# Kernel optimization log

Hardware: AMD Instinct MI355X
Metric: run time of the kernel (lower is better)

Reference implementation:

```python
import jax, jax.numpy as jnp
import numpy as np

D = 768; HID = 3072; FFN = 2048; NH = 8; NL = 2; T = 64; V = 50257; B = 16
ALPHA = 0.4; HD = D // NH

def _gelu(x):
    return jax.nn.gelu(x, approximate=False)

def _ln(x, g, b, eps=1e-5):
    m = x.mean(-1, keepdims=True)
    v = x.var(-1, keepdims=True)
    return (x - m) / jnp.sqrt(v + eps) * g + b

def _l2norm(x):
    return x / jnp.maximum(jnp.linalg.norm(x, axis=-1, keepdims=True), 1e-12)

def _mha(x, in_w, in_b, out_w, out_b, mask):
    b, t, _ = x.shape
    qkv = x @ in_w.T + in_b
    q, k, v = jnp.split(qkv, 3, axis=-1)
    q = q.reshape(b, t, NH, HD); k = k.reshape(b, t, NH, HD); v = v.reshape(b, t, NH, HD)
    s = jnp.einsum('bqhd,bkhd->bhqk', q, k) / jnp.sqrt(jnp.asarray(HD, jnp.float32))
    s = jnp.where(mask[None, None], -jnp.inf, s)
    a = jax.nn.softmax(s, axis=-1)
    o = jnp.einsum('bhqk,bkhd->bqhd', a, v).reshape(b, t, D)
    return o @ out_w.T + out_b

def _forward(token_ids, emb, pos_emb, attn_in_w, attn_in_b, attn_out_w, attn_out_b,
             ff_w1, ff_b1, ff_w2, ff_b2, n1_g, n1_b, n2_g, n2_b, enc_norm_g, enc_norm_b,
             V0, b0, V1, b1, cp_w1, cp_b1, cp_w2, cp_b2, gate_w, gate_b, temp_w, R,
             out_g, out_b, lm_head):
    sg = jax.lax.stop_gradient
    x = emb[token_ids] + pos_emb[None, :token_ids.shape[1]]
    t = token_ids.shape[1]
    mask = jnp.triu(jnp.ones((t, t), bool), 1)
    for l in range(NL):
        xn = _ln(x, n1_g[l], n1_b[l])
        x = x + _mha(xn, attn_in_w[l], attn_in_b[l], attn_out_w[l], attn_out_b[l], mask)
        xn = _ln(x, n2_g[l], n2_b[l])
        x = x + _gelu(xn @ ff_w1[l].T + ff_b1[l]) @ ff_w2[l].T + ff_b2[l]
    ctx = _l2norm(_ln(x, enc_norm_g, enc_norm_b))  # [B,T,D]

    def step(h_prev, ctx_t):
        h_d = sg(h_prev)                      # h_prev.detach()
        traw = h_d @ R                        # temporal_raw
        tc = ctx_t + ALPHA * traw             # temporal_context
        # differentiable shadow path through hierarchy weights V0,b0,V1,b1
        h_sh = _gelu(tc @ V0 + b0)
        core_sh = _l2norm(_gelu(h_sh @ V1 + b1))
        # settled state: hierarchy inference under no_grad (settle approximated
        # by the same feedforward pass; fully stop-gradiented like x.detach())
        tcd = sg(tc)
        core_set = sg(_l2norm(_gelu(_gelu(tcd @ V0 + b0) @ V1 + b1)))
        blend = 0.5 * core_sh + 0.5 * core_set
        cf = _gelu(blend @ cp_w1.T + cp_b1) @ cp_w2.T + cp_b2   # core_proj
        tf = traw @ temp_w.T                                     # temporal_proj
        gate = jax.nn.sigmoid(jnp.concatenate([ctx_t, cf], -1) @ gate_w.T + gate_b)
        h_t = gate * (cf + ALPHA * tf) + (1.0 - gate) * ctx_t    # gate_warmup=1.0
        h_t = jnp.clip(_ln(h_t, out_g, out_b), -5.0, 5.0)
        return sg(h_t), h_t @ lm_head.T

    h0 = jnp.zeros((token_ids.shape[0], D), jnp.float32)
    _, logits = jax.lax.scan(step, h0, jnp.swapaxes(ctx, 0, 1))
    return jnp.transpose(logits, (1, 0, 2))

def setup_inputs():
    key = jax.random.key(0)
    ks = iter(jax.random.split(key, 64))
    def nrm(shape, s=0.02):
        return jax.random.normal(next(ks), shape, jnp.float32) * s
    return {
        'token_ids': jax.random.randint(next(ks), (B, T), 0, V),
        'emb': nrm((V, D)),
        'pos_emb': nrm((T, D)),
        'attn_in_w': nrm((NL, 3 * D, D)),
        'attn_in_b': jnp.zeros((NL, 3 * D), jnp.float32),
        'attn_out_w': nrm((NL, D, D)),
        'attn_out_b': jnp.zeros((NL, D), jnp.float32),
        'ff_w1': nrm((NL, FFN, D)),
        'ff_b1': jnp.zeros((NL, FFN), jnp.float32),
        'ff_w2': nrm((NL, D, FFN)),
        'ff_b2': jnp.zeros((NL, D), jnp.float32),
        'n1_g': jnp.ones((NL, D), jnp.float32),
        'n1_b': jnp.zeros((NL, D), jnp.float32),
        'n2_g': jnp.ones((NL, D), jnp.float32),
        'n2_b': jnp.zeros((NL, D), jnp.float32),
        'enc_norm_g': jnp.ones((D,), jnp.float32),
        'enc_norm_b': jnp.zeros((D,), jnp.float32),
        'V0': nrm((D, HID)),
        'b0': jnp.zeros((HID,), jnp.float32),
        'V1': nrm((HID, D)),
        'b1': jnp.zeros((D,), jnp.float32),
        'cp_w1': nrm((D, D)),
        'cp_b1': jnp.zeros((D,), jnp.float32),
        'cp_w2': nrm((D, D)),
        'cp_b2': jnp.zeros((D,), jnp.float32),
        'gate_w': nrm((D, 2 * D)),
        'gate_b': jnp.zeros((D,), jnp.float32),
        'temp_w': nrm((D, D)),
        'R': nrm((D, D), 0.1),
        'out_g': jnp.ones((D,), jnp.float32),
        'out_b': jnp.zeros((D,), jnp.float32),
        'lm_head': nrm((V, D)),
    }

def reference(token_ids, emb, pos_emb, attn_in_w, attn_in_b, attn_out_w, attn_out_b,
              ff_w1, ff_b1, ff_w2, ff_b2, n1_g, n1_b, n2_g, n2_b, enc_norm_g, enc_norm_b,
              V0, b0, V1, b1, cp_w1, cp_b1, cp_w2, cp_b2, gate_w, gate_b, temp_w, R,
              out_g, out_b, lm_head):
    return _forward(token_ids, emb, pos_emb, attn_in_w, attn_in_b, attn_out_w, attn_out_b,
                    ff_w1, ff_b1, ff_w2, ff_b2, n1_g, n1_b, n2_g, n2_b, enc_norm_g, enc_norm_b,
                    V0, b0, V1, b1, cp_w1, cp_b1, cp_w2, cp_b2, gate_w, gate_b, temp_w, R,
                    out_g, out_b, lm_head)
```

## Files before the change

### kernel.cpp

```cpp
#include <hip/hip_runtime.h>
#include <math.h>

typedef _Float16 f16;
typedef f16 f16x8 __attribute__((ext_vector_type(8)));
typedef f16 f16x4 __attribute__((ext_vector_type(4)));
typedef float f32x4 __attribute__((ext_vector_type(4)));
typedef unsigned int u32;
typedef unsigned long long u64;

#define TT 64
#define DD 768
#define MR 1024
#define ALPHAF 0.4f
#define NWG 120
#define GRID 240
#define LMN 50257
#define LMK 768

__device__ __forceinline__ float geluf(float x){
  return 0.5f*x*(1.0f + erff(x*0.70710678118654752f));
}

__device__ __forceinline__ u64 ld_a64(const void* p){
  return __hip_atomic_load((const u64*)p, __ATOMIC_RELAXED, __HIP_MEMORY_SCOPE_AGENT);
}
__device__ __forceinline__ f16x8 ld_act16h(const f16* p){
  union { u64 u[2]; f16x8 v; } c;
  c.u[0] = ld_a64(p); c.u[1] = ld_a64(p + 4); return c.v;
}
__device__ __forceinline__ float ld_actf(const float* p){
  union { u32 u; float f; } c;
  c.u = __hip_atomic_load((const u32*)p, __ATOMIC_RELAXED, __HIP_MEMORY_SCOPE_AGENT);
  return c.f;
}
__device__ __forceinline__ void st_actf(float* p, float v){
  union { u32 u; float f; } c; c.f = v;
  __hip_atomic_store((u32*)p, c.u, __ATOMIC_RELAXED, __HIP_MEMORY_SCOPE_AGENT);
}
__device__ __forceinline__ void st_acth(f16* p, float v){
  union { unsigned short u; f16 h; } c; c.h = (f16)v;
  __hip_atomic_store((unsigned short*)p, c.u, __ATOMIC_RELAXED, __HIP_MEMORY_SCOPE_AGENT);
}

__device__ __forceinline__ void egbar(int* ef, int ep){
  __syncthreads();
  if (threadIdx.x == 0){
    __threadfence();
    __hip_atomic_store(ef + blockIdx.x*32, ep, __ATOMIC_RELAXED, __HIP_MEMORY_SCOPE_AGENT);
  }
  {
    int id = threadIdx.x; bool active = id < GRID;
    const int* fp = ef + id*32;
    while (true){
      int v = active ? __hip_atomic_load(fp, __ATOMIC_RELAXED, __HIP_MEMORY_SCOPE_AGENT) : ep;
      if (__ballot(v >= ep) == ~0ull) break;
      __builtin_amdgcn_s_sleep(1);
    }
  }
  __syncthreads();
  if (threadIdx.x == 0) __threadfence();
  __syncthreads();
}

__device__ __forceinline__ void postf(int* f, int ep){
  asm volatile("s_waitcnt vmcnt(0)" ::: "memory");
  __syncthreads();
  if (threadIdx.x == 0)
    __hip_atomic_store(f, ep, __ATOMIC_RELAXED, __HIP_MEMORY_SCOPE_AGENT);
}
__device__ __forceinline__ void waitf(const int* f, int n, int ep){
  if (threadIdx.x < 64){
    int lane = threadIdx.x;
    while (true){
      bool ok = true;
      for (int i = lane; i < n; i += 64){
        if (__hip_atomic_load(f + i*32, __ATOMIC_RELAXED, __HIP_MEMORY_SCOPE_AGENT) < ep){
          ok = false; break;
        }
      }
      if (__ballot(ok) == ~0ull) break;
      __builtin_amdgcn_s_sleep(1);
    }
  }
  __syncthreads();
}

__device__ __forceinline__ void red_store(float* rb, int lane, f32x4 a){
  rb[lane] = a[0]; rb[64+lane] = a[1]; rb[128+lane] = a[2]; rb[192+lane] = a[3];
}
__device__ __forceinline__ f32x4 red_sum4(float rb[4][256], int lane){
  f32x4 s;
  #pragma unroll
  for (int r = 0; r < 4; r++)
    s[r] = rb[0][r*64+lane] + rb[1][r*64+lane] + rb[2][r*64+lane] + rb[3][r*64+lane];
  return s;
}
__device__ __forceinline__ f32x4 red_sum2(float rb[4][256], int lane, int w0, int w1){
  f32x4 s;
  #pragma unroll
  for (int r = 0; r < 4; r++)
    s[r] = rb[w0][r*64+lane] + rb[w1][r*64+lane];
  return s;
}

__device__ void dev_ln(const float* xr, const float* g, const float* b,
                       float* outr, float* outTr, float* red, bool l2n){
  int tid = threadIdx.x, lane = tid & 63, wid = tid >> 6;
  float v[3]; float s = 0.f, ss = 0.f;
  #pragma unroll
  for (int j = 0; j < 3; j++){ float t0 = xr[tid + j*256]; v[j] = t0; s += t0; ss += t0*t0; }
  #pragma unroll
  for (int o = 1; o < 64; o <<= 1){ s += __shfl_xor(s, o); ss += __shfl_xor(ss, o); }
  if (lane == 0){ red[wid] = s; red[4+wid] = ss; }
  __syncthreads();
  s  = red[0]+red[1]+red[2]+red[3];
  ss = red[4]+red[5]+red[6]+red[7];
  float mean = s*(1.f/768.f);
  float var  = ss*(1.f/768.f) - mean*mean;
  float rstd = rsqrtf(var + 1e-5f);
  float y[3];
  #pragma unroll
  for (int j = 0; j < 3; j++){ int n = tid + j*256; y[j] = (v[j]-mean)*rstd*g[n] + b[n]; }
  if (l2n){
    float n2 = y[0]*y[0] + y[1]*y[1] + y[2]*y[2];
    #pragma unroll
    for (int o = 1; o < 64; o <<= 1) n2 += __shfl_xor(n2, o);
    __syncthreads();
    if (lane == 0) red[wid] = n2;
    __syncthreads();
    n2 = red[0]+red[1]+red[2]+red[3];
    float inv = 1.f / fmaxf(sqrtf(n2), 1e-12f);
    y[0] *= inv; y[1] *= inv; y[2] *= inv;
  }
  #pragma unroll
  for (int j = 0; j < 3; j++) outr[tid + j*256] = y[j];
  if (outTr){
    #pragma unroll
    for (int j = 0; j < 3; j++) outTr[tid + j*256] = y[j];
  }
  __syncthreads();
}

__device__ void dev_gemm_tile(char* lds, const float* A, int lda,
    const float* Bw, int ldb, int nrb, int N, int K, int m0, int n0,
    const float* bias, const float* res, float* outF, f16* outH,
    float scale, int act, int operm)
{
  int tid = threadIdx.x;
  int lane = tid & 63, wid = tid >> 6;
  int wr = (wid >> 1)*64, wc = (wid & 1)*64;
  int l15 = lane & 15, kb = lane >> 4;
  f32x4 acc[4][4];
  #pragma unroll
  for (int i = 0; i < 4; i++)
    #pragma unroll
    for (int j = 0; j < 4; j++){ f32x4 z = {0.f,0.f,0.f,0.f}; acc[i][j] = z; }
  int rA = tid >> 3;
  int k4 = (tid & 7)*4;
  float4 va[4], vb[4];
  #pragma unroll
  for (int it = 0; it < 4; ++it){
    int r = it*32 + rA;
    va[it] = *(const float4*)(A + (size_t)(m0+r)*lda + k4);
    int rB = n0 + r;
    if (rB < nrb) vb[it] = *(const float4*)(Bw + (size_t)rB*ldb + k4);
    else { vb[it].x=0.f; vb[it].y=0.f; vb[it].z=0.f; vb[it].w=0.f; }
  }
  for (int kk = 0; kk < K; kk += 32){
    char* cb = lds + (((kk >> 5) & 1) ? 20480 : 0);
    f16 (*As)[40] = (f16(*)[40])cb;
    f16 (*Bs)[40] = (f16(*)[40])(cb + 10240);
    #pragma unroll
    for (int it = 0; it < 4; ++it){
      int r = it*32 + rA;
      *(f16x4*)(&As[r][k4]) = (f16x4){(f16)va[it].x,(f16)va[it].y,(f16)va[it].z,(f16)va[it].w};
      *(f16x4*)(&Bs[r][k4]) = (f16x4){(f16)vb[it].x,(f16)vb[it].y,(f16)vb[it].z,(f16)vb[it].w};
    }
    __syncthreads();
    if (kk + 32 < K){
      #pragma unroll
      for (int it = 0; it < 4; ++it){
        int r = it*32 + rA;
        va[it] = *(const float4*)(A + (size_t)(m0+r)*lda + kk + 32 + k4);
        int rB = n0 + r;
        if (rB < nrb) vb[it] = *(const float4*)(Bw + (size_t)rB*ldb + kk + 32 + k4);
        else { vb[it].x=0.f; vb[it].y=0.f; vb[it].z=0.f; vb[it].w=0.f; }
      }
    }
    f16x8 af[4], bfv[4];
    #pragma unroll
    for (int i = 0; i < 4; i++) af[i]  = *(const f16x8*)(&As[wr + i*16 + l15][kb*8]);
    #pragma unroll
    for (int j = 0; j < 4; j++) bfv[j] = *(const f16x8*)(&Bs[wc + j*16 + l15][kb*8]);
    #pragma unroll
    for (int i = 0; i < 4; i++)
      #pragma unroll
      for (int j = 0; j < 4; j++)
        acc[i][j] = __builtin_amdgcn_mfma_f32_16x16x32_f16(af[i], bfv[j], acc[i][j], 0, 0, 0);
  }
  __syncthreads();
  #pragma unroll
  for (int i = 0; i < 4; i++){
    #pragma unroll
    for (int j = 0; j < 4; j++){
      #pragma unroll
      for (int r = 0; r < 4; r++){
        int m = m0 + wr + i*16 + kb*4 + r;
        int n = n0 + wc + j*16 + l15;
        if (n < N){
          float v = acc[i][j][r]*scale;
          if (bias) v += bias[n];
          if (act == 1) v = geluf(v);
          if (res) v += res[(size_t)m*N + n];
          size_t off;
          if (operm == 0) off = (size_t)m*N + n;
          else            off = ((size_t)(m & 63)*16 + (m >> 6))*N + n;
          if (outF) outF[off] = v;
          if (outH) outH[off] = (f16)v;
        }
      }
    }
  }
}

__device__ void dev_attn(char* lds, const float* qkv, float* o, int bh){
  float (*kv)[96] = (float(*)[96])lds;
  float (*sm)[68] = (float(*)[68])(lds + 24576);
  int b = bh >> 3, h = bh & 7;
  int tid = threadIdx.x;
  const float* base = qkv + (size_t)b*64*2304 + h*96;
  for (int idx = tid; idx < 64*96; idx += 256){ int i = idx/96, d = idx - i*96;
    kv[i][d] = base[(size_t)i*2304 + 768 + d]; }
  __syncthreads();
  {
    int i = tid >> 2;
    const float* q = base + (size_t)i*2304;
    int j0 = (tid & 3)*16;
    for (int jj = 0; jj < 16; jj++){
      int j = j0 + jj;
      float sv = -1e30f;
      if (j <= i){ float acc = 0.f;
        for (int d = 0; d < 96; d++) acc += q[d]*kv[j][d];
        sv = acc*0.10206207261596576f; }
      sm[i][j] = sv;
    }
  }
  __syncthreads();
  for (int idx = tid; idx < 64*96; idx += 256){ int i = idx/96, d = idx - i*96;
    kv[i][d] = base[(size_t)i*2304 + 1536 + d]; }
  if (tid < 64){
    int i = tid;
    float mx = -1e30f;
    for (int j = 0; j <= i; j++) mx = fmaxf(mx, sm[i][j]);
    float sum = 0.f;
    for (int j = 0; j <= i; j++){ float e = expf(sm[i][j]-mx); sm[i][j] = e; sum += e; }
    float inv = 1.f/sum;
    for (int j = 0; j <= i; j++) sm[i][j] *= inv;
  }
  __syncthreads();
  for (int idx = tid; idx < 64*96; idx += 256){
    int i = idx/96, d = idx - i*96;
    float acc = 0.f;
    for (int j = 0; j <= i; j++) acc += sm[i][j]*kv[j][d];
    o[(size_t)(b*64+i)*768 + h*96 + d] = acc;
  }
  __syncthreads();
}

__device__ void dev_tr_f(char* lds, const float* in, float* out, int R, int C, int bx, int by){
  float (*tile)[33] = (float(*)[33])lds;
  int r0 = by*32, c0 = bx*32;
  int tx = threadIdx.x & 31, ty = threadIdx.x >> 5;
  #pragma unroll
  for (int i = 0; i < 32; i += 8) tile[ty+i][tx] = in[(size_t)(r0+ty+i)*C + (c0+tx)];
  __syncthreads();
  #pragma unroll
  for (int i = 0; i < 32; i += 8) out[(size_t)(c0+ty+i)*R + (r0+tx)] = tile[tx][ty+i];
  __syncthreads();
}
__device__ void dev_tr_h(char* lds, const float* in, f16* out, int R, int C, int bx, int by){
  float (*tile)[33] = (float(*)[33])lds;
  int r0 = by*32, c0 = bx*32;
  int tx = threadIdx.x & 31, ty = threadIdx.x >> 5;
  #pragma unroll
  for (int i = 0; i < 32; i += 8) tile[ty+i][tx] = in[(size_t)(r0+ty+i)*C + (c0+tx)];
  __syncthreads();
  #pragma unroll
  for (int i = 0; i < 32; i += 8) out[(size_t)(c0+ty+i)*R + (r0+tx)] = (f16)tile[tx][ty+i];
  __syncthreads();
}

__global__ void k_init(int* flags){
  for (int i = threadIdx.x; i < 512*32; i += 256) flags[i] = 0;
}

__global__ __launch_bounds__(256, 1) void k_all(
  const int* tok, const float* emb, const float* pos,
  const float* aiw, const float* aib, const float* aow, const float* aob,
  const float* fw1, const float* fb1, const float* fw2, const float* fb2,
  const float* n1g, const float* n1b, const float* n2g, const float* n2b,
  const float* eng, const float* enb,
  const float* V0, const float* b0, const float* V1, const float* b1,
  const float* cw1, const float* cb1, const float* cw2, const float* cb2,
  const float* gw, const float* gb_, const float* tw, const float* Rm,
  const float* og, const float* ob, const float* lmw,
  float* x, float* xn, float* qkv, float* o_, float* mid,
  float* ctx, float* ctxT, float* V0t, float* cw2t,
  float* ctxV0T, float* gctxT, float* bdg,
  f16* WAf, f16* V1tf, f16* Wc1f, f16* WDf, f16* lmw16,
  f16* hf, f16* h1f, f16* c1f, f16* gcaf,
  float* cf, float* gpre, float* tfs, int* flags, float* out)
{
  __shared__ __align__(16) char smem[147456];
  __shared__ float redbuf[4][256];
  __shared__ float normp[4][16];
  __shared__ float red[8];
  const int tid = threadIdx.x, lane = tid & 63, wid = tid >> 6;
  const int bid = blockIdx.x;
  const int l15 = lane & 15, kb = lane >> 4;
  int* afl = flags;
  int* bfl = flags + 120*32;
  int* cfl = flags + 168*32;
  int* dfl = flags + 192*32;
  int* mfl = flags + 240*32;
  int* encf = flags + 256*32;
  int eep = 0;

  for (int m = bid; m < MR; m += GRID){
    int t = m & 63; int id = tok[m];
    const float* e = emb + (size_t)id*DD;
    const float* p = pos + (size_t)t*DD;
    float* xr = x + (size_t)m*DD;
    for (int j = tid; j < DD; j += 256) xr[j] = e[j] + p[j];
  }
  egbar(encf, ++eep);

  for (int l = 0; l < 2; l++){
    for (int m = bid; m < MR; m += GRID)
      dev_ln(x + (size_t)m*DD, n1g + l*DD, n1b + l*DD, xn + (size_t)m*DD, nullptr, red, false);
    egbar(encf, ++eep);
    for (int tl = bid; tl < 144; tl += GRID)
      dev_gemm_tile(smem, xn, 768, aiw + (size_t)l*2304*768, 768, 2304, 2304, 768,
                    (tl % 8)*128, (tl / 8)*128, aib + l*2304, nullptr, qkv, nullptr, 1.f, 0, 0);
    egbar(encf, ++eep);
    for (int u = bid; u < 128; u += GRID) dev_attn(smem, qkv, o_, u);
    egbar(encf, ++eep);
    for (int tl = bid; tl < 48; tl += GRID)
      dev_gemm_tile(smem, o_, 768, aow + (size_t)l*768*768, 768, 768, 768, 768,
                    (tl % 8)*128, (tl / 8)*128, aob + l*768, x, x, nullptr, 1.f, 0, 0);
    egbar(encf, ++eep);
    for (int m = bid; m < MR; m += GRID)
      dev_ln(x + (size_t)m*DD, n2g + l*DD, n2b + l*DD, xn + (size_t)m*DD, nullptr, red, false);
    egbar(encf, ++eep);
    for (int tl = bid; tl < 128; tl += GRID)
      dev_gemm_tile(smem, xn, 768, fw1 + (size_t)l*2048*768, 768, 2048, 2048, 768,
                    (tl % 8)*128, (tl / 8)*128, fb1 + l*2048, nullptr, mid, nullptr, 1.f, 1, 0);
    egbar(encf, ++eep);
    for (int tl = bid; tl < 48; tl += GRID)
      dev_gemm_tile(smem, mid, 2048, fw2 + (size_t)l*768*2048, 2048, 768, 768, 2048,
                    (tl % 8)*128, (tl / 8)*128, fb2 + l*768, x, x, nullptr, 1.f, 0, 0);
    egbar(encf, ++eep);
  }
  for (int m = bid; m < MR; m += GRID)
    dev_ln(x + (size_t)m*DD, eng, enb, ctx + (size_t)m*DD,
           ctxT + ((size_t)(m & 63)*16 + (m >> 6))*DD, red, true);
  egbar(encf, ++eep);

  for (int task = bid; task < 5184; task += GRID){
    if (task < 2304)      dev_tr_f(smem, V0, V0t, 768, 3072, task % 96, task / 96);
    else if (task < 2880){ int t2 = task - 2304; dev_tr_f(smem, cw2, cw2t, 768, 768, t2 % 24, t2 / 24); }
    else                 { int t2 = task - 2880; dev_tr_h(smem, V1, V1tf, 3072, 768, t2 % 24, t2 / 24); }
  }
  {
    const int g0 = bid*256 + tid, stride = GRID*256;
    for (int i = g0; i < 73728; i += stride){
      float4 a = ((const float4*)cw1)[i*2]; float4 b2 = ((const float4*)cw1)[i*2+1];
      ((f16x8*)Wc1f)[i] = (f16x8){(f16)a.x,(f16)a.y,(f16)a.z,(f16)a.w,(f16)b2.x,(f16)b2.y,(f16)b2.z,(f16)b2.w};
    }
    for (int i = g0; i < 73728; i += stride){
      float4 a = ((const float4*)cw2)[i*2]; float4 b2 = ((const float4*)cw2)[i*2+1];
      ((f16x8*)WDf)[i] = (f16x8){(f16)a.x,(f16)a.y,(f16)a.z,(f16)a.w,(f16)b2.x,(f16)b2.y,(f16)b2.z,(f16)b2.w};
    }
    for (int g = g0; g < 768; g += stride){
      const float* row = gw + (size_t)g*1536 + 768;
      float s = 0.f;
      for (int j = 0; j < 768; j++) s += cb2[j]*row[j];
      bdg[g] = s;
    }
  }
  egbar(encf, ++eep);

  for (int task = bid; task < 456; task += GRID){
    if (task < 144)
      dev_gemm_tile(smem, V0t, 768, Rm, 768, 768, 768, 768,
                    (task % 24)*128, (task / 24)*128, nullptr, nullptr, nullptr, WAf, ALPHAF, 0, 0);
    else if (task < 180){ int t2 = task - 144;
      dev_gemm_tile(smem, tw, 768, Rm, 768, 768, 768, 768,
                    (t2 % 6)*128, (t2 / 6)*128, nullptr, nullptr, nullptr, WAf + (size_t)3072*768, ALPHAF, 0, 0); }
    else if (task < 372){ int t2 = task - 180;
      dev_gemm_tile(smem, ctx, 768, V0t, 768, 3072, 3072, 768,
                    (t2 % 8)*128, (t2 / 8)*128, b0, nullptr, ctxV0T, nullptr, 1.f, 0, 1); }
    else if (task < 420){ int t2 = task - 372;
      dev_gemm_tile(smem, ctx, 768, gw, 1536, 768, 768, 768,
                    (t2 % 8)*128, (t2 / 8)*128, nullptr, nullptr, gctxT, nullptr, 1.f, 0, 1); }
    else { int t2 = task - 420;
      dev_gemm_tile(smem, gw + 768, 1536, cw2t, 768, 768, 768, 768,
                    (t2 % 6)*128, (t2 / 6)*128, nullptr, nullptr, nullptr, WDf + (size_t)768*768, 1.f, 0, 0); }
  }
  egbar(encf, ++eep);

  if (bid >= NWG){
    const int lw = bid - NWG;
    const int wr = (wid >> 1)*64, wc = (wid & 1)*64;
    for (int nt = lw; nt < 393; nt += 120){
      int r0 = nt*128;
      int rend = r0 + 128; if (rend > LMN) rend = LMN;
      int u0 = r0*96, u1 = rend*96;
      for (int i = u0 + tid; i < u1; i += 256){
        float4 a = ((const float4*)lmw)[(size_t)i*2];
        float4 b2 = ((const float4*)lmw)[(size_t)i*2+1];
        ((f16x8*)lmw16)[i] = (f16x8){(f16)a.x,(f16)a.y,(f16)a.z,(f16)a.w,
                                     (f16)b2.x,(f16)b2.y,(f16)b2.z,(f16)b2.w};
      }
    }
    __syncthreads();
    for (int q = 0; q < 8; ++q){
      waitf(mfl, 16, q*8 + 8);
      size_t arow[4];
      #pragma unroll
      for (int i = 0; i < 4; i++){
        int rl = wr + i*16 + l15;
        arow[i] = ((size_t)(rl >> 3)*TT + q*8 + (rl & 7))*DD + kb*8;
      }
      for (int nt = lw; nt < 393; nt += 120){
        int n0 = nt*128;
        size_t brow[4];
        #pragma unroll
        for (int j = 0; j < 4; j++){
          int n = n0 + wc + j*16 + l15;
          if (n > LMN-1) n = LMN-1;
          brow[j] = (size_t)n*LMK + kb*8;
        }
        f32x4 acc[4][4];
        #pragma unroll
        for (int i = 0; i < 4; i++)
          #pragma unroll
          for (int j = 0; j < 4; j++){ f32x4 z = {0.f,0.f,0.f,0.f}; acc[i][j] = z; }
        #pragma unroll 4
        for (int kk = 0; kk < LMK; kk += 32){
          f16x8 af[4], bf[4];
          #pragma unroll
          for (int i = 0; i < 4; i++) af[i] = ld_act16h(hf + arow[i] + kk);
          #pragma unroll
          for (int j = 0; j < 4; j++) bf[j] = *(const f16x8*)(lmw16 + brow[j] + kk);
          #pragma unroll
          for (int i = 0; i < 4; i++)
            #pragma unroll
            for (int j = 0; j < 4; j++)
              acc[i][j] = __builtin_amdgcn_mfma_f32_16x16x32_f16(af[i], bf[j], acc[i][j], 0, 0, 0);
        }
        #pragma unroll
        for (int i = 0; i < 4; i++){
          #pragma unroll
          for (int j = 0; j < 4; j++){
            #pragma unroll
            for (int r = 0; r < 4; r++){
              int ml = wr + i*16 + kb*4 + r;
              int b = ml >> 3, tt = q*8 + (ml & 7);
              int n = n0 + wc + j*16 + l15;
              if (n < LMN) out[((size_t)b*TT + tt)*LMN + n] = acc[i][j][r];
            }
          }
        }
      }
    }
    return;
  }

  {
    const f16* src = WAf + (size_t)bid*32*768;
    for (int c = tid; c < 3072; c += 256){
      int row = c/96, kc = c - row*96;
      int off = (row*1536 + kc*16) ^ ((row&7)<<4);
      *(f16x8*)(smem + off) = *(const f16x8*)(src + (size_t)row*768 + kc*8);
    }
    if (bid < 48){
      const f16* s2 = V1tf + (size_t)bid*16*3072;
      for (int c = tid; c < 6144; c += 256){
        int row = c/384, kc = c - row*384;
        int off = (row*6144 + kc*16) ^ ((row&7)<<4);
        *(f16x8*)(smem + 49152 + off) = *(const f16x8*)(s2 + (size_t)row*3072 + kc*8);
      }
    } else if (bid < 72){
      const f16* s2 = Wc1f + (size_t)(bid-48)*32*768;
      for (int c = tid; c < 3072; c += 256){
        int row = c/96, kc = c - row*96;
        int off = (row*1536 + kc*16) ^ ((row&7)<<4);
        *(f16x8*)(smem + 49152 + off) = *(const f16x8*)(s2 + (size_t)row*768 + kc*8);
      }
    } else {
      const f16* s2 = WDf + (size_t)(bid-72)*32*768;
      for (int c = tid; c < 3072; c += 256){
        int row = c/96, kc = c - row*96;
        int off = (row*1536 + kc*16) ^ ((row&7)<<4);
        *(f16x8*)(smem + 49152 + off) = *(const f16x8*)(s2 + (size_t)row*768 + kc*8);
      }
    }
  }
  __syncthreads();

  const int n_a = bid*32 + (wid>>1)*16 + l15;
  float b1v = 0.f;
  if (bid < 48) b1v = b1[bid*16 + l15];
  float cpb1v = 0.f;
  if (bid >= 48 && bid < 72) cpb1v = cb1[((bid-48)*2 + (wid>>1))*16 + l15];
  float dbv = 0.f; int n_d = 0;
  if (bid >= 72){
    n_d = ((bid-72)*2 + (wid>>1))*16 + l15;
    dbv = (n_d < 768) ? cb2[n_d] : bdg[n_d - 768];
  }
  float gb3[3], og3[3], ob3[3];
  if (bid < 16){
    #pragma unroll
    for (int j = 0; j < 3; j++){
      int n = tid + j*256;
      gb3[j] = gb_[n]; og3[j] = og[n]; ob3[j] = ob[n];
    }
  }

  for (int t = 0; t < TT; ++t){
    const int ep = t + 1;
    f32x4 cv = {0.f,0.f,0.f,0.f};
    if ((wid & 1) == 0 && n_a < 3072){
      const float* p = ctxV0T + (size_t)t*16*3072 + n_a;
      #pragma unroll
      for (int r = 0; r < 4; r++) cv[r] = p[(size_t)(kb*4+r)*3072];
    }

    if (t > 0) waitf(mfl, 16, t);
    {
      const int u = wid >> 1, kh = wid & 1;
      const int k0 = kh*384 + kb*8;
      f32x4 a = {0.f,0.f,0.f,0.f};
      if (t > 0){
        const f16* ap = hf + ((size_t)l15*TT + (t-1))*DD + k0;
        const int row = u*16 + l15, rowoff = row*1536, sw = (row&7)<<4;
        #pragma unroll
        for (int b = 0; b < 12; b++){
          int wb = (rowoff + (k0 + b*32)*2) ^ sw;
          f16x8 vb = *(const f16x8*)(smem + wb);
          f16x8 va = ld_act16h(ap + b*32);
          a = __builtin_amdgcn_mfma_f32_16x16x32_f16(va, vb, a, 0,0,0);
        }
      }
      red_store(redbuf[wid], lane, a);
    }
    __syncthreads();
    if ((wid & 1) == 0){
      f32x4 s4 = red_sum2(redbuf, lane, wid, wid+1);
      #pragma unroll
      for (int r = 0; r < 4; r++){
        int m = kb*4 + r;
        if (n_a < 3072){
          float hv = geluf(s4[r] + cv[r]);
          st_acth(h1f + (size_t)m*3072 + n_a, hv);
        } else {
          st_actf(tfs + m*DD + (n_a - 3072), s4[r]);
        }
      }
    }
    postf(afl + bid*32, ep);
    if (bid < 48){
      waitf(afl, 120, ep);
      const int k0 = wid*768 + kb*8;
      const f16* ap = h1f + (size_t)l15*3072 + k0;
      const int rowoff = l15*6144, sw = (l15&7)<<4;
      f32x4 a = {0.f,0.f,0.f,0.f};
      #pragma unroll
      for (int b = 0; b < 24; b++){
        int wb = (rowoff + (k0 + b*32)*2) ^ sw;
        f16x8 vb = *(const f16x8*)(smem + 49152 + wb);
        f16x8 va = ld_act16h(ap + b*32);
        a = __builtin_amdgcn_mfma_f32_16x16x32_f16(va, vb, a, 0,0,0);
      }
      red_store(redbuf[wid], lane, a);
      __syncthreads();
      if (wid == 0){
        f32x4 s4 = red_sum4(redbuf, lane);
        int n = bid*16 + l15;
        #pragma unroll
        for (int r = 0; r < 4; r++){
          int m = kb*4 + r;
          st_acth(c1f + (size_t)m*DD + n, geluf(s4[r] + b1v));
        }
      }
      postf(bfl + bid*32, ep);
    }
    float gv[3], cxv[3];
    if (bid < 16){
      #pragma unroll
      for (int j = 0; j < 3; j++){
        size_t o2 = ((size_t)t*16 + bid)*DD + tid + j*256;
        gv[j] = gctxT[o2]; cxv[j] = ctxT[o2];
      }
    }
    if (bid >= 48 && bid < 72){
      waitf(bfl, 48, ep);
      const int u = wid >> 1, kh = wid & 1;
      const int k0 = kh*384 + kb*8;
      const f16* ap = c1f + (size_t)l15*DD + k0;
      const int row = u*16 + l15, rowoff = row*1536, sw = (row&7)<<4;
      f32x4 a = {0.f,0.f,0.f,0.f};
      float sq = 0.f;
      #pragma unroll
      for (int b = 0; b < 12; b++){
        int wb = (rowoff + (k0 + b*32)*2) ^ sw;
        f16x8 vb = *(const f16x8*)(smem + 49152 + wb);
        f16x8 va = ld_act16h(ap + b*32);
        a = __builtin_amdgcn_mfma_f32_16x16x32_f16(va, vb, a, 0,0,0);
        #pragma unroll
        for (int j = 0; j < 8; j++){ float xv = (float)va[j]; sq = fmaf(xv, xv, sq); }
      }
      sq += __shfl_xor(sq,16); sq += __shfl_xor(sq,32);
      if (lane < 16) normp[wid][lane] = sq;
      red_store(redbuf[wid], lane, a);
      __syncthreads();
      if ((wid & 1) == 0){
        f32x4 s4 = red_sum2(redbuf, lane, wid, wid+1);
        int n = ((bid-48)*2 + (wid>>1))*16 + l15;
        #pragma unroll
        for (int r = 0; r < 4; r++){
          int m = kb*4 + r;
          float nm = normp[wid][m] + normp[wid+1][m];
          float inv = 1.f / fmaxf(sqrtf(nm), 1e-12f);
          st_acth(gcaf + (size_t)m*DD + n, geluf(s4[r]*inv + cpb1v));
        }
      }
      postf(cfl + (bid-48)*32, ep);
    }
    if (bid >= 72){
      waitf(cfl, 24, ep);
      const int u = wid >> 1, kh = wid & 1;
      const int k0 = kh*384 + kb*8;
      const f16* ap = gcaf + (size_t)l15*DD + k0;
      const int row = u*16 + l15, rowoff = row*1536, sw = (row&7)<<4;
      f32x4 a = {0.f,0.f,0.f,0.f};
      #pragma unroll
      for (int b = 0; b < 12; b++){
        int wb = (rowoff + (k0 + b*32)*2) ^ sw;
        f16x8 vb = *(const f16x8*)(smem + 49152 + wb);
        f16x8 va = ld_act16h(ap + b*32);
        a = __builtin_amdgcn_mfma_f32_16x16x32_f16(va, vb, a, 0,0,0);
      }
      red_store(redbuf[wid], lane, a);
      __syncthreads();
      if ((wid & 1) == 0){
        f32x4 s4 = red_sum2(redbuf, lane, wid, wid+1);
        #pragma unroll
        for (int r = 0; r < 4; r++){
          int m = kb*4 + r;
          if (n_d < 768) st_actf(cf + m*DD + n_d, s4[r] + dbv);
          else           st_actf(gpre + m*DD + (n_d - 768), s4[r] + dbv);
        }
      }
      postf(dfl + (bid-72)*32, ep);
    }
    if (bid < 16){
      waitf(dfl, 48, ep);
      int m = bid;
      float vals[3]; float s = 0.f, ss = 0.f;
      #pragma unroll
      for (int j = 0; j < 3; j++){
        int n = tid + j*256;
        float gi = gv[j] + ld_actf(gpre + m*DD + n) + gb3[j];
        float gate = 1.f/(1.f + expf(-gi));
        float v = gate*(ld_actf(cf + m*DD + n) + ld_actf(tfs + m*DD + n)) + (1.f - gate)*cxv[j];
        vals[j] = v; s += v; ss += v*v;
      }
      #pragma unroll
      for (int o2 = 1; o2 < 64; o2 <<= 1){ s += __shfl_xor(s, o2); ss += __shfl_xor(ss, o2); }
      if (lane == 0){ red[wid] = s; red[4+wid] = ss; }
      __syncthreads();
      s  = red[0]+red[1]+red[2]+red[3];
      ss = red[4]+red[5]+red[6]+red[7];
      float mean = s*(1.f/768.f), var = ss*(1.f/768.f) - mean*mean;
      float rstd = rsqrtf(var + 1e-5f);
      #pragma unroll
      for (int j = 0; j < 3; j++){
        int n = tid + j*256;
        float y = (vals[j]-mean)*rstd*og3[j] + ob3[j];
        y = fminf(5.f, fmaxf(-5.f, y));
        st_acth(hf + ((size_t)m*TT + t)*DD + n, y);
      }
      postf(mfl + bid*32, ep);
    }
  }
}

extern "C" void kernel_launch(void* const* d_in, const int* in_sizes, int n_in,
                              void* d_out, int out_size, void* d_ws, size_t ws_size,
                              hipStream_t stream)
{
  (void)in_sizes; (void)n_in; (void)out_size; (void)ws_size;
  const int*   tok = (const int*)d_in[0];
  const float* emb = (const float*)d_in[1];
  const float* pos = (const float*)d_in[2];
  const float* aiw = (const float*)d_in[3];
  const float* aib = (const float*)d_in[4];
  const float* aow = (const float*)d_in[5];
  const float* aob = (const float*)d_in[6];
  const float* fw1 = (const float*)d_in[7];
  const float* fb1 = (const float*)d_in[8];
  const float* fw2 = (const float*)d_in[9];
  const float* fb2 = (const float*)d_in[10];
  const float* n1g = (const float*)d_in[11];
  const float* n1b = (const float*)d_in[12];
  const float* n2g = (const float*)d_in[13];
  const float* n2b = (const float*)d_in[14];
  const float* eng = (const float*)d_in[15];
  const float* enb = (const float*)d_in[16];
  const float* V0  = (const float*)d_in[17];
  const float* b0  = (const float*)d_in[18];
  const float* V1  = (const float*)d_in[19];
  const float* b1  = (const float*)d_in[20];
  const float* cw1 = (const float*)d_in[21];
  const float* cb1 = (const float*)d_in[22];
  const float* cw2 = (const float*)d_in[23];
  const float* cb2 = (const float*)d_in[24];
  const float* gw  = (const float*)d_in[25];
  const float* gb  = (const float*)d_in[26];
  const float* tw  = (const float*)d_in[27];
  const float* Rm  = (const float*)d_in[28];
  const float* og  = (const float*)d_in[29];
  const float* ob  = (const float*)d_in[30];
  const float* lmw = (const float*)d_in[31];
  float* out = (float*)d_out;

  char* base = (char*)d_ws; size_t off = 0;
  auto alloc = [&](size_t bytes)->void*{
    off = (off + 255) & ~(size_t)255; void* p = base + off; off += bytes; return p; };

  float* x     = (float*)alloc((size_t)MR*DD*4);
  float* xn    = (float*)alloc((size_t)MR*DD*4);
  float* qkv   = (float*)alloc((size_t)MR*2304*4);
  float* o_    = (float*)alloc((size_t)MR*DD*4);
  float* mid   = (float*)alloc((size_t)MR*2048*4);
  float* ctx   = (float*)alloc((size_t)MR*DD*4);
  float* ctxT  = (float*)alloc((size_t)MR*DD*4);
  float* V0t   = (float*)alloc((size_t)3072*768*4);
  float* cw2t  = (float*)alloc((size_t)768*768*4);
  float* ctxV0T= (float*)alloc((size_t)MR*3072*4);
  float* gctxT = (float*)alloc((size_t)MR*DD*4);
  float* bdg   = (float*)alloc(768*4);
  f16*   WAf   = (f16*)alloc((size_t)3840*768*2);
  f16*   V1tf  = (f16*)alloc((size_t)768*3072*2);
  f16*   Wc1f  = (f16*)alloc((size_t)768*768*2);
  f16*   WDf   = (f16*)alloc((size_t)1536*768*2);
  f16*   lmw16 = (f16*)alloc((size_t)LMN*768*2);
  f16*   hf    = (f16*)alloc((size_t)MR*DD*2);
  f16*   h1f   = (f16*)alloc((size_t)16*3072*2);
  f16*   c1f   = (f16*)alloc((size_t)16*768*2);
  f16*   gcaf  = (f16*)alloc((size_t)16*768*2);
  float* cf    = (float*)alloc((size_t)16*768*4);
  float* gpre  = (float*)alloc((size_t)16*768*4);
  float* tfs   = (float*)alloc((size_t)16*768*4);
  int*   flags = (int*)alloc((size_t)512*32*4);

  k_init<<<1, 256, 0, stream>>>(flags);
  k_all<<<GRID, 256, 0, stream>>>(tok, emb, pos, aiw, aib, aow, aob,
      fw1, fb1, fw2, fb2, n1g, n1b, n2g, n2b, eng, enb,
      V0, b0, V1, b1, cw1, cb1, cw2, cb2, gw, gb, tw, Rm, og, ob, lmw,
      x, xn, qkv, o_, mid, ctx, ctxT, V0t, cw2t, ctxV0T, gctxT, bdg,
      WAf, V1tf, Wc1f, WDf, lmw16, hf, h1f, c1f, gcaf, cf, gpre, tfs, flags, out);
}
```

Measured before the change: 2.698 ms.

## Fuse LayerNorm into GEMM A-loads and split-K the FFN down-projection

Replaces the materialized LayerNorm passes with per-row mean/rstd statistics, which are applied while loading A tiles in the QKV and FFN1 GEMMs. Stats for the first LN are computed during embedding. The FFN2 GEMM is split four ways over K into partial buffers, giving 192 tiles instead of 48 to fill the 240-block grid. A finish pass sums the partials with the residual and bias, computes the next stats, and for the last layer folds in the final norm plus L2 normalization. It also changes one flag index in the recurrent phase from block id to row id. The intent is fewer grid barriers and less xn traffic, at the cost of extra partial-sum memory traffic and per-element normalize work inside the GEMM load loop.

```diff
diff --git a/kernel.cpp b/kernel.cpp
--- a/kernel.cpp
+++ b/kernel.cpp
@@ -103,12 +103,11 @@
   return s;
 }
 
-__device__ void dev_ln(const float* xr, const float* g, const float* b,
-                       float* outr, float* outTr, float* red, bool l2n){
+__device__ void dev_rowstats(const float* xr, float* red, float2* outstat){
   int tid = threadIdx.x, lane = tid & 63, wid = tid >> 6;
-  float v[3]; float s = 0.f, ss = 0.f;
-  #pragma unroll
-  for (int j = 0; j < 3; j++){ float t0 = xr[tid + j*256]; v[j] = t0; s += t0; ss += t0*t0; }
+  float s = 0.f, ss = 0.f;
+  #pragma unroll
+  for (int j = 0; j < 3; j++){ float t0 = xr[tid + j*256]; s += t0; ss += t0*t0; }
   #pragma unroll
   for (int o = 1; o < 64; o <<= 1){ s += __shfl_xor(s, o); ss += __shfl_xor(ss, o); }
   if (lane == 0){ red[wid] = s; red[4+wid] = ss; }
@@ -116,27 +115,56 @@
   s  = red[0]+red[1]+red[2]+red[3];
   ss = red[4]+red[5]+red[6]+red[7];
   float mean = s*(1.f/768.f);
-  float var  = ss*(1.f/768.f) - mean*mean;
-  float rstd = rsqrtf(var + 1e-5f);
+  float rstd = rsqrtf(ss*(1.f/768.f) - mean*mean + 1e-5f);
+  if (tid == 0){ outstat->x = mean; outstat->y = rstd; }
+  __syncthreads();
+}
+
+__device__ void dev_ff2_finish(const float* pfb, const float* bias, float* x, int m,
+    float* red, float2* outstat, bool finalln,
+    const float* g, const float* b, float* ctx, float* ctxT){
+  int tid = threadIdx.x, lane = tid & 63, wid = tid >> 6;
+  float* xr = x + (size_t)m*DD;
+  float v[3]; float s = 0.f, ss = 0.f;
+  #pragma unroll
+  for (int j = 0; j < 3; j++){
+    int n = tid + j*256;
+    size_t o = (size_t)m*DD + n;
+    float t0 = xr[n] + bias[n] + pfb[o] + pfb[(size_t)MR*DD + o]
+             + pfb[2*(size_t)MR*DD + o] + pfb[3*(size_t)MR*DD + o];
+    xr[n] = t0; v[j] = t0; s += t0; ss += t0*t0;
+  }
+  #pragma unroll
+  for (int o = 1; o < 64; o <<= 1){ s += __shfl_xor(s, o); ss += __shfl_xor(ss, o); }
+  if (lane == 0){ red[wid] = s; red[4+wid] = ss; }
+  __syncthreads();
+  s  = red[0]+red[1]+red[2]+red[3];
+  ss = red[4]+red[5]+red[6]+red[7];
+  float mean = s*(1.f/768.f);
+  float rstd = rsqrtf(ss*(1.f/768.f) - mean*mean + 1e-5f);
+  if (!finalln){
+    if (tid == 0){ outstat->x = mean; outstat->y = rstd; }
+    __syncthreads();
+    return;
+  }
   float y[3];
   #pragma unroll
   for (int j = 0; j < 3; j++){ int n = tid + j*256; y[j] = (v[j]-mean)*rstd*g[n] + b[n]; }
-  if (l2n){
-    float n2 = y[0]*y[0] + y[1]*y[1] + y[2]*y[2];
-    #pragma unroll
-    for (int o = 1; o < 64; o <<= 1) n2 += __shfl_xor(n2, o);
-    __syncthreads();
-    if (lane == 0) red[wid] = n2;
-    __syncthreads();
-    n2 = red[0]+red[1]+red[2]+red[3];
-    float inv = 1.f / fmaxf(sqrtf(n2), 1e-12f);
-    y[0] *= inv; y[1] *= inv; y[2] *= inv;
-  }
-  #pragma unroll
-  for (int j = 0; j < 3; j++) outr[tid + j*256] = y[j];
-  if (outTr){
-    #pragma unroll
-    for (int j = 0; j < 3; j++) outTr[tid + j*256] = y[j];
+  float n2 = y[0]*y[0] + y[1]*y[1] + y[2]*y[2];
+  #pragma unroll
+  for (int o = 1; o < 64; o <<= 1) n2 += __shfl_xor(n2, o);
+  __syncthreads();
+  if (lane == 0) red[wid] = n2;
+  __syncthreads();
+  n2 = red[0]+red[1]+red[2]+red[3];
+  float inv = 1.f / fmaxf(sqrtf(n2), 1e-12f);
+  float* cT = ctxT + ((size_t)(m & 63)*16 + (m >> 6))*DD;
+  #pragma unroll
+  for (int j = 0; j < 3; j++){
+    int n = tid + j*256;
+    float yy = y[j]*inv;
+    ctx[(size_t)m*DD + n] = yy;
+    cT[n] = yy;
   }
   __syncthreads();
 }
@@ -144,7 +172,8 @@
 __device__ void dev_gemm_tile(char* lds, const float* A, int lda,
     const float* Bw, int ldb, int nrb, int N, int K, int m0, int n0,
     const float* bias, const float* res, float* outF, f16* outH,
-    float scale, int act, int operm)
+    float scale, int act, int operm,
+    const float2* lnstats, const float* lng, const float* lnb)
 {
   int tid = threadIdx.x;
   int lane = tid & 63, wid = tid >> 6;
@@ -157,7 +186,14 @@
     for (int j = 0; j < 4; j++){ f32x4 z = {0.f,0.f,0.f,0.f}; acc[i][j] = z; }
   int rA = tid >> 3;
   int k4 = (tid & 7)*4;
+  float2 msr[4];
+  if (lnstats){
+    #pragma unroll
+    for (int it = 0; it < 4; ++it) msr[it] = lnstats[m0 + it*32 + rA];
+  }
   float4 va[4], vb[4];
+  float4 g4, b4;
+  if (lnstats){ g4 = *(const float4*)(lng + k4); b4 = *(const float4*)(lnb + k4); }
   #pragma unroll
   for (int it = 0; it < 4; ++it){
     int r = it*32 + rA;
@@ -166,6 +202,16 @@
     if (rB < nrb) vb[it] = *(const float4*)(Bw + (size_t)rB*ldb + k4);
     else { vb[it].x=0.f; vb[it].y=0.f; vb[it].z=0.f; vb[it].w=0.f; }
   }
+  if (lnstats){
+    #pragma unroll
+    for (int it = 0; it < 4; ++it){
+      float mn = msr[it].x, rs = msr[it].y;
+      va[it].x = (va[it].x-mn)*rs*g4.x + b4.x;
+      va[it].y = (va[it].y-mn)*rs*g4.y + b4.y;
+      va[it].z = (va[it].z-mn)*rs*g4.z + b4.z;
+      va[it].w = (va[it].w-mn)*rs*g4.w + b4.w;
+    }
+  }
   for (int kk = 0; kk < K; kk += 32){
     char* cb = lds + (((kk >> 5) & 1) ? 20480 : 0);
     f16 (*As)[40] = (f16(*)[40])cb;
@@ -178,6 +224,7 @@
     }
     __syncthreads();
     if (kk + 32 < K){
+      if (lnstats){ g4 = *(const float4*)(lng + kk + 32 + k4); b4 = *(const float4*)(lnb + kk + 32 + k4); }
       #pragma unroll
       for (int it = 0; it < 4; ++it){
         int r = it*32 + rA;
@@ -185,6 +232,16 @@
         int rB = n0 + r;
         if (rB < nrb) vb[it] = *(const float4*)(Bw + (size_t)rB*ldb + kk + 32 + k4);
         else { vb[it].x=0.f; vb[it].y=0.f; vb[it].z=0.f; vb[it].w=0.f; }
+      }
+      if (lnstats){
+        #pragma unroll
+        for (int it = 0; it < 4; ++it){
+          float mn = msr[it].x, rs = msr[it].y;
+          va[it].x = (va[it].x-mn)*rs*g4.x + b4.x;
+          va[it].y = (va[it].y-mn)*rs*g4.y + b4.y;
+          va[it].z = (va[it].z-mn)*rs*g4.z + b4.z;
+          va[it].w = (va[it].w-mn)*rs*g4.w + b4.w;
+        }
       }
     }
     f16x8 af[4], bfv[4];
@@ -304,9 +361,10 @@
   const float* cw1, const float* cb1, const float* cw2, const float* cb2,
   const float* gw, const float* gb_, const float* tw, const float* Rm,
   const float* og, const float* ob, const float* lmw,
-  float* x, float* xn, float* qkv, float* o_, float* mid,
+  float* x, float* qkv, float* o_, float* mid,
   float* ctx, float* ctxT, float* V0t, float* cw2t,
   float* ctxV0T, float* gctxT, float* bdg,
+  float2* stats, float* pfb,
   f16* WAf, f16* V1tf, f16* Wc1f, f16* WDf, f16* lmw16,
   f16* hf, f16* h1f, f16* c1f, f16* gcaf,
   float* cf, float* gpre, float* tfs, int* flags, float* out)
@@ -331,40 +389,58 @@
     const float* e = emb + (size_t)id*DD;
     const float* p = pos + (size_t)t*DD;
     float* xr = x + (size_t)m*DD;
-    for (int j = tid; j < DD; j += 256) xr[j] = e[j] + p[j];
+    float s = 0.f, ss = 0.f;
+    #pragma unroll
+    for (int j = 0; j < 3; j++){
+      int n = tid + j*256;
+      float t0 = e[n] + p[n];
+      xr[n] = t0; s += t0; ss += t0*t0;
+    }
+    #pragma unroll
+    for (int o2 = 1; o2 < 64; o2 <<= 1){ s += __shfl_xor(s, o2); ss += __shfl_xor(ss, o2); }
+    if (lane == 0){ red[wid] = s; red[4+wid] = ss; }
+    __syncthreads();
+    s  = red[0]+red[1]+red[2]+red[3];
+    ss = red[4]+red[5]+red[6]+red[7];
+    float mean = s*(1.f/768.f);
+    float rstd = rsqrtf(ss*(1.f/768.f) - mean*mean + 1e-5f);
+    if (tid == 0){ stats[m].x = mean; stats[m].y = rstd; }
+    __syncthreads();
   }
   egbar(encf, ++eep);
 
   for (int l = 0; l < 2; l++){
-    for (int m = bid; m < MR; m += GRID)
-      dev_ln(x + (size_t)m*DD, n1g + l*DD, n1b + l*DD, xn + (size_t)m*DD, nullptr, red, false);
-    egbar(encf, ++eep);
     for (int tl = bid; tl < 144; tl += GRID)
-      dev_gemm_tile(smem, xn, 768, aiw + (size_t)l*2304*768, 768, 2304, 2304, 768,
-                    (tl % 8)*128, (tl / 8)*128, aib + l*2304, nullptr, qkv, nullptr, 1.f, 0, 0);
+      dev_gemm_tile(smem, x, 768, aiw + (size_t)l*2304*768, 768, 2304, 2304, 768,
+                    (tl % 8)*128, (tl / 8)*128, aib + l*2304, nullptr, qkv, nullptr, 1.f, 0, 0,
+                    stats, n1g + l*DD, n1b + l*DD);
     egbar(encf, ++eep);
     for (int u = bid; u < 128; u += GRID) dev_attn(smem, qkv, o_, u);
     egbar(encf, ++eep);
     for (int tl = bid; tl < 48; tl += GRID)
       dev_gemm_tile(smem, o_, 768, aow + (size_t)l*768*768, 768, 768, 768, 768,
-                    (tl % 8)*128, (tl / 8)*128, aob + l*768, x, x, nullptr, 1.f, 0, 0);
+                    (tl % 8)*128, (tl / 8)*128, aob + l*768, x, x, nullptr, 1.f, 0, 0,
+                    nullptr, nullptr, nullptr);
+    egbar(encf, ++eep);
+    for (int m = bid; m < MR; m += GRID) dev_rowstats(x + (size_t)m*DD, red, stats + m);
+    egbar(encf, ++eep);
+    for (int tl = bid; tl < 128; tl += GRID)
+      dev_gemm_tile(smem, x, 768, fw1 + (size_t)l*2048*768, 768, 2048, 2048, 768,
+                    (tl % 8)*128, (tl / 8)*128, fb1 + l*2048, nullptr, mid, nullptr, 1.f, 1, 0,
+                    stats, n2g + l*DD, n2b + l*DD);
+    egbar(encf, ++eep);
+    for (int t2 = bid; t2 < 192; t2 += GRID){
+      int tl = t2 >> 2, ks = t2 & 3;
+      dev_gemm_tile(smem, mid + ks*512, 2048, fw2 + (size_t)l*768*2048 + ks*512, 2048, 768, 768, 512,
+                    (tl % 8)*128, (tl / 8)*128, nullptr, nullptr,
+                    pfb + (size_t)ks*MR*DD, nullptr, 1.f, 0, 0,
+                    nullptr, nullptr, nullptr);
+    }
     egbar(encf, ++eep);
     for (int m = bid; m < MR; m += GRID)
-      dev_ln(x + (size_t)m*DD, n2g + l*DD, n2b + l*DD, xn + (size_t)m*DD, nullptr, red, false);
+      dev_ff2_finish(pfb, fb2 + l*DD, x, m, red, stats + m, (l == 1), eng, enb, ctx, ctxT);
     egbar(encf, ++eep);
-    for (int tl = bid; tl < 128; tl += GRID)
-      dev_gemm_tile(smem, xn, 768, fw1 + (size_t)l*2048*768, 768, 2048, 2048, 768,
-                    (tl % 8)*128, (tl / 8)*128, fb1 + l*2048, nullptr, mid, nullptr, 1.f, 1, 0);
-    egbar(encf, ++eep);
-    for (int tl = bid; tl < 48; tl += GRID)
-      dev_gemm_tile(smem, mid, 2048, fw2 + (size_t)l*768*2048, 2048, 768, 768, 2048,
-                    (tl % 8)*128, (tl / 8)*128, fb2 + l*768, x, x, nullptr, 1.f, 0, 0);
-    egbar(encf, ++eep);
-  }
-  for (int m = bid; m < MR; m += GRID)
-    dev_ln(x + (size_t)m*DD, eng, enb, ctx + (size_t)m*DD,
-           ctxT + ((size_t)(m & 63)*16 + (m >> 6))*DD, red, true);
-  egbar(encf, ++eep);
+  }
 
   for (int task = bid; task < 5184; task += GRID){
     if (task < 2304)      dev_tr_f(smem, V0, V0t, 768, 3072, task % 96, task / 96);
@@ -393,19 +469,24 @@
   for (int task = bid; task < 456; task += GRID){
     if (task < 144)
       dev_gemm_tile(smem, V0t, 768, Rm, 768, 768, 768, 768,
-                    (task % 24)*128, (task / 24)*128, nullptr, nullptr, nullptr, WAf, ALPHAF, 0, 0);
+                    (task % 24)*128, (task / 24)*128, nullptr, nullptr, nullptr, WAf, ALPHAF, 0, 0,
+                    nullptr, nullptr, nullptr);
     else if (task < 180){ int t2 = task - 144;
       dev_gemm_tile(smem, tw, 768, Rm, 768, 768, 768, 768,
-                    (t2 % 6)*128, (t2 / 6)*128, nullptr, nullptr, nullptr, WAf + (size_t)3072*768, ALPHAF, 0, 0); }
+                    (t2 % 6)*128, (t2 / 6)*128, nullptr, nullptr, nullptr, WAf + (size_t)3072*768, ALPHAF, 0, 0,
+                    nullptr, nullptr, nullptr); }
     else if (task < 372){ int t2 = task - 180;
       dev_gemm_tile(smem, ctx, 768, V0t, 768, 3072, 3072, 768,
-                    (t2 % 8)*128, (t2 / 8)*128, b0, nullptr, ctxV0T, nullptr, 1.f, 0, 1); }
+                    (t2 % 8)*128, (t2 / 8)*128, b0, nullptr, ctxV0T, nullptr, 1.f, 0, 1,
+                    nullptr, nullptr, nullptr); }
     else if (task < 420){ int t2 = task - 372;
       dev_gemm_tile(smem, ctx, 768, gw, 1536, 768, 768, 768,
-                    (t2 % 8)*128, (t2 / 8)*128, nullptr, nullptr, gctxT, nullptr, 1.f, 0, 1); }
+                    (t2 % 8)*128, (t2 / 8)*128, nullptr, nullptr, gctxT, nullptr, 1.f, 0, 1,
+                    nullptr, nullptr, nullptr); }
     else { int t2 = task - 420;
       dev_gemm_tile(smem, gw + 768, 1536, cw2t, 768, 768, 768, 768,
-                    (t2 % 6)*128, (t2 / 6)*128, nullptr, nullptr, nullptr, WDf + (size_t)768*768, 1.f, 0, 0); }
+                    (t2 % 6)*128, (t2 / 6)*128, nullptr, nullptr, nullptr, WDf + (size_t)768*768, 1.f, 0, 0,
+                    nullptr, nullptr, nullptr); }
   }
   egbar(encf, ++eep);
 
@@ -460,18 +541,16 @@
               acc[i][j] = __builtin_amdgcn_mfma_f32_16x16x32_f16(af[i], bf[j], acc[i][j], 0, 0, 0);
         }
         #pragma unroll
-        for (int i = 0; i < 4; i++){
+        for (int i = 0; i < 4; i++)
           #pragma unroll
-          for (int j = 0; j < 4; j++){
+          for (int j = 0; j < 4; j++)
             #pragma unroll
             for (int r = 0; r < 4; r++){
               int ml = wr + i*16 + kb*4 + r;
-              int b = ml >> 3, tt = q*8 + (ml & 7);
+              int b = ml >> 3, tt2 = q*8 + (ml & 7);
               int n = n0 + wc + j*16 + l15;
-              if (n < LMN) out[((size_t)b*TT + tt)*LMN + n] = acc[i][j][r];
+              if (n < LMN) out[((size_t)b*TT + tt2)*LMN + n] = acc[i][j][r];
             }
-          }
-        }
       }
     }
     return;
@@ -692,7 +771,7 @@
         y = fminf(5.f, fmaxf(-5.f, y));
         st_acth(hf + ((size_t)m*TT + t)*DD + n, y);
       }
-      postf(mfl + bid*32, ep);
+      postf(mfl + m*32, ep);
     }
   }
 }
@@ -741,7 +820,6 @@
     off = (off + 255) & ~(size_t)255; void* p = base + off; off += bytes; return p; };
 
   float* x     = (float*)alloc((size_t)MR*DD*4);
-  float* xn    = (float*)alloc((size_t)MR*DD*4);
   float* qkv   = (float*)alloc((size_t)MR*2304*4);
   float* o_    = (float*)alloc((size_t)MR*DD*4);
   float* mid   = (float*)alloc((size_t)MR*2048*4);
@@ -752,6 +830,8 @@
   float* ctxV0T= (float*)alloc((size_t)MR*3072*4);
   float* gctxT = (float*)alloc((size_t)MR*DD*4);
   float* bdg   = (float*)alloc(768*4);
+  float2* stats= (float2*)alloc((size_t)MR*8);
+  float* pfb   = (float*)alloc((size_t)4*MR*DD*4);
   f16*   WAf   = (f16*)alloc((size_t)3840*768*2);
   f16*   V1tf  = (f16*)alloc((size_t)768*3072*2);
   f16*   Wc1f  = (f16*)alloc((size_t)768*768*2);
@@ -770,6 +850,6 @@
   k_all<<<GRID, 256, 0, stream>>>(tok, emb, pos, aiw, aib, aow, aob,
       fw1, fb1, fw2, fb2, n1g, n1b, n2g, n2b, eng, enb,
       V0, b0, V1, b1, cw1, cb1, cw2, cb2, gw, gb, tw, Rm, og, ob, lmw,
-      x, xn, qkv, o_, mid, ctx, ctxT, V0t, cw2t, ctxV0T, gctxT, bdg,
+      x, qkv, o_, mid, ctx, ctxT, V0t, cw2t, ctxV0T, gctxT, bdg, stats, pfb,
       WAf, V1tf, Wc1f, WDf, lmw16, hf, h1f, c1f, gcaf, cf, gpre, tfs, flags, out);
 }
```

New measurement: 2.600 ms. 1.04x faster.
